# Kernel tuning notes

Measured on AMD Instinct MI355X. Metric: run time of the kernel, lower is better.

Reference implementation:

```python
import jax, jax.numpy as jnp
import numpy as np
from jax.scipy.special import gammaln, xlogy

DIM = 1536
HEADS = 8
DK = 64
DV = 64
BS = 128
N = 1536
NRPF = 192  # num_rel_pos_features, divisible by 6
B = 2


def _positional_embed(n, feat):
    # [2n-1, feat] relative positional basis (exponential, central-mask, gamma),
    # each duplicated with sign(d) asymmetric variant.
    f = feat // 6
    d = jnp.arange(-n + 1, n, dtype=jnp.float32)
    ad = jnp.abs(d)[:, None]  # [2n-1, 1]
    # exponential: log-spaced half lives
    half_life = 2.0 ** jnp.linspace(3.0, float(np.log2(n)), f)
    e_exp = jnp.exp(-float(np.log(2.0)) / half_life[None, :] * ad)
    # central mask: 1 if |d| < 2^i - 1
    widths = 2.0 ** jnp.arange(1, f + 1, dtype=jnp.float32) - 1.0
    e_cm = (widths[None, :] > ad).astype(jnp.float32)
    # gamma pdf, linearly spaced means
    std = n / (2.0 * f)
    mean = jnp.linspace(n / f, float(n), f)[None, :]
    conc = (mean / std) ** 2
    rate = mean / (std ** 2)
    log_unnorm = xlogy(conc - 1.0, ad) - rate * ad
    log_norm = gammaln(conc) - conc * jnp.log(rate)
    probs = jnp.exp(log_unnorm - log_norm) + 1e-8
    e_g = probs / jnp.max(probs, axis=-1, keepdims=True)
    emb = jnp.concatenate([e_exp, e_cm, e_g], axis=-1)  # [2n-1, 3f]
    return jnp.concatenate([emb, jnp.sign(d)[:, None] * emb], axis=-1)  # [2n-1, 6f]


def _relative_shift(t):
    # [B, H, N, 2N-1] -> [B, H, N, N] (Transformer-XL shift)
    b, h, t1, t2 = t.shape
    t = jnp.concatenate([jnp.zeros_like(t[..., :1]), t], axis=-1)  # [.., t2+1]
    t = t.reshape(b, h, t2 + 1, t1)[:, :, 1:, :].reshape(b, h, t1, t2)
    return t[..., :t1]


def setup_inputs() -> dict:
    key = jax.random.key(0)
    ks = jax.random.split(key, 10)
    x = jax.random.normal(ks[0], (B, N, DIM), dtype=jnp.float32)
    Wq = jax.random.normal(ks[1], (DIM, HEADS * DK), dtype=jnp.float32) * 0.02
    Wk = jax.random.normal(ks[2], (DIM, HEADS * DK), dtype=jnp.float32) * 0.02
    Wv = jax.random.normal(ks[3], (DIM, HEADS * DV), dtype=jnp.float32) * 0.02
    Wrel = jax.random.normal(ks[4], (NRPF, HEADS * DK), dtype=jnp.float32) * 0.02
    rel_content_bias = jax.random.normal(ks[5], (1, HEADS, 1, DK), dtype=jnp.float32)
    rel_pos_bias = jax.random.normal(ks[6], (1, HEADS, 1, DK), dtype=jnp.float32)
    # to_out is zero-init in the original; use small random so the output/grads are non-trivial
    Wo = jax.random.normal(ks[7], (HEADS * DV, DIM), dtype=jnp.float32) * 0.02
    bo = jnp.zeros((DIM,), dtype=jnp.float32)
    pos_embed = _positional_embed(N, NRPF)  # [2N-1, NRPF]
    # BigBird block-local window mask: blocks bi attend to blocks bi-1..bi+1
    bi = np.arange(N) // BS
    local_mask = jnp.asarray(np.abs(bi[:, None] - bi[None, :]) <= 1)  # [N, N] bool
    # a few global tokens per batch
    is_global = jnp.zeros((B, N), dtype=bool).at[:, :4].set(True)
    return {"x": x, "Wq": Wq, "Wk": Wk, "Wv": Wv, "Wrel": Wrel,
            "rel_content_bias": rel_content_bias, "rel_pos_bias": rel_pos_bias,
            "Wo": Wo, "bo": bo, "pos_embed": pos_embed,
            "local_mask": local_mask, "is_global": is_global}


def reference(x, Wq, Wk, Wv, Wrel, rel_content_bias, rel_pos_bias, Wo, bo,
              pos_embed, local_mask, is_global):
    b, n, _ = x.shape
    h, dk = rel_content_bias.shape[1], rel_content_bias.shape[-1]
    dv = Wv.shape[-1] // h
    scale = dk ** -0.5
    q = (x @ Wq).reshape(b, n, h, dk).transpose(0, 2, 1, 3) * scale  # [b,h,n,dk]
    k = (x @ Wk).reshape(b, n, h, dk).transpose(0, 2, 1, 3)
    v = (x @ Wv).reshape(b, n, h, dv).transpose(0, 2, 1, 3)
    content_logits = jnp.einsum('bhid,bhjd->bhij', q + rel_content_bias, k)
    rel_k = (pos_embed @ Wrel).reshape(2 * n - 1, h, dk).transpose(1, 0, 2)  # [h,2n-1,dk]
    rel_logits = jnp.einsum('bhid,hjd->bhij', q + rel_pos_bias, rel_k)  # [b,h,n,2n-1]
    logits = content_logits + _relative_shift(rel_logits)
    attn_bool = (local_mask[None, None] | is_global[:, None, :, None]
                 | is_global[:, None, None, :])
    logits = jnp.where(attn_bool, logits.astype(jnp.float32), -jnp.inf)
    attn = jax.nn.softmax(logits, axis=-1)
    out = jnp.einsum('bhij,bhjd->bhid', attn, v.astype(jnp.float32))
    out = out.astype(x.dtype).transpose(0, 2, 1, 3).reshape(b, n, h * dv)
    return out @ Wo + bo
```

## Files before the change

kernel.cpp:

```cpp
#include <hip/hip_runtime.h>
#include <math.h>

#define NSEQ 1536
#define HD3  1536
#define RKLD 512
#define RLEN 3071
#define NB   12

typedef __attribute__((ext_vector_type(8))) short bf16x8;
typedef __attribute__((ext_vector_type(4))) float f32x4;
typedef _Float16 f16x8 __attribute__((ext_vector_type(8)));
typedef _Float16 f16x4 __attribute__((ext_vector_type(4)));

__device__ __forceinline__ unsigned short f2bf(float f) {
    union { float f; unsigned u; } v; v.f = f;
    unsigned r = v.u + 0x7fffu + ((v.u >> 16) & 1u);
    return (unsigned short)(r >> 16);
}
__device__ __forceinline__ float bf2f(unsigned short s) {
    union { unsigned u; float f; } v; v.u = ((unsigned)s) << 16;
    return v.f;
}
__device__ __forceinline__ unsigned short f2h(float f) {
    union { _Float16 h; unsigned short u; } c; c.h = (_Float16)f; return c.u;
}
__device__ __forceinline__ void cp16(const void* g, void* l) {
    __builtin_amdgcn_global_load_lds(
        (const __attribute__((address_space(1))) void*)g,
        (__attribute__((address_space(3))) void*)l, 16, 0, 0);
}

#define KSWZ(row, d) ((row) * 64 + (((((d) >> 3) ^ ((row) & 7))) << 3) + ((d) & 7))
#define PSWZ(r, j)   ((r) * 128 + (((((j) >> 3) ^ ((r) & 15))) << 3) + ((j) & 7))
#define VSTR 136

__global__ __launch_bounds__(256) void split2_f16(
    const float* __restrict__ X, _Float16* __restrict__ HX,
    const float* __restrict__ P, _Float16* __restrict__ HP)
{
    const int bid = blockIdx.x;
    const float* src; _Float16* dst; int i;
    if (bid < 4608) {
        i = bid * 256 + threadIdx.x;
        src = X; dst = HX;
    } else {
        i = (bid - 4608) * 256 + threadIdx.x;
        if (i >= 147408) return;
        src = P; dst = HP;
    }
    float4 v = ((const float4*)src)[i];
    union { _Float16 h[4]; ushort4 u; } c;
    c.h[0] = (_Float16)v.x; c.h[1] = (_Float16)v.y;
    c.h[2] = (_Float16)v.z; c.h[3] = (_Float16)v.w;
    ((ushort4*)dst)[i] = c.u;
}

__device__ __forceinline__ void wsplit_body16(
    const float* __restrict__ W, _Float16* __restrict__ T,
    int K, int N, int n_off, int ldt, float scale, int bx, int by)
{
    __shared__ float tile[64][65];
    const int k0 = by * 64, n0 = bx * 64;
    const int t = threadIdx.x;
    const int rr = t >> 4, c4 = (t & 15) * 4;
#pragma unroll
    for (int p = 0; p < 4; ++p) {
        int r = p * 16 + rr;
        float4 v = *(const float4*)(W + (size_t)(k0 + r) * N + n0 + c4);
        tile[r][c4 + 0] = v.x; tile[r][c4 + 1] = v.y;
        tile[r][c4 + 2] = v.z; tile[r][c4 + 3] = v.w;
    }
    __syncthreads();
#pragma unroll
    for (int p = 0; p < 4; ++p) {
        int n = p * 16 + rr;
        union { _Float16 h[4]; ushort4 u; } cc;
        cc.h[0] = (_Float16)(tile[c4 + 0][n] * scale);
        cc.h[1] = (_Float16)(tile[c4 + 1][n] * scale);
        cc.h[2] = (_Float16)(tile[c4 + 2][n] * scale);
        cc.h[3] = (_Float16)(tile[c4 + 3][n] * scale);
        size_t o = (size_t)(n_off + n0 + n) * ldt + k0 + c4;
        *(ushort4*)(T + o) = cc.u;
    }
}

__global__ __launch_bounds__(256) void wsplit_all(
    const float* __restrict__ Wq, const float* __restrict__ Wk,
    const float* __restrict__ Wv, const float* __restrict__ Wo,
    const float* __restrict__ Wrel,
    _Float16* __restrict__ Tqkv, _Float16* __restrict__ To,
    _Float16* __restrict__ Trel)
{
    const int z = blockIdx.z;
    if (z < 3) {
        const float* W = (z == 0) ? Wq : (z == 1) ? Wk : Wv;
        wsplit_body16(W, Tqkv, 1536, 512, z * 512, 1536,
                      (z == 0) ? 0.125f : 1.f, blockIdx.x, blockIdx.y);
    } else if (z == 3) {
        wsplit_body16(Wo, To, 512, 1536, 0, 512, 1.f, blockIdx.y, blockIdx.x);
    } else {
        if (blockIdx.y >= 3) return;
        wsplit_body16(Wrel, Trel, 192, 512, 0, 192, 1.f, blockIdx.x, blockIdx.y);
    }
}

__global__ __launch_bounds__(256) void gemm_f16k(
    const _Float16* __restrict__ A,
    const _Float16* __restrict__ B,
    const float* __restrict__ bias, void* __restrict__ C,
    int M, int N, int K, int omode)
{
    __shared__ _Float16 sA[2][4096];
    __shared__ _Float16 sB[2][4096];
    const int t = threadIdx.x;
    const int wave = t >> 6, lane = t & 63;
    const int nwg = gridDim.x * gridDim.y;
    const int lin = blockIdx.y * gridDim.x + blockIdx.x;
    const int swz = (lin & 7) * (nwg >> 3) + (lin >> 3);
    const int bx = swz % gridDim.x, by = swz / gridDim.x;
    const int m0 = by * 64, n0 = bx * 64;
    const int wm = (wave >> 1) * 32, wn = (wave & 1) * 32;
    const int fr = lane & 15, quad = lane >> 4;

    f32x4 acc[2][2];
#pragma unroll
    for (int i = 0; i < 2; ++i)
#pragma unroll
        for (int j = 0; j < 2; ++j)
#pragma unroll
            for (int c = 0; c < 4; ++c) acc[i][j][c] = 0.f;

    const int nsteps = K >> 6;

#define STAGE(k0, buf)                                                        \
    {                                                                         \
        _Pragma("unroll")                                                     \
        for (int it = 0; it < 2; ++it) {                                      \
            int cidx = it * 256 + t;                                          \
            int row = cidx >> 3, slot = cidx & 7;                             \
            int gch = slot ^ (row & 7);                                       \
            size_t goA = (size_t)(m0 + row) * K + (k0) + gch * 8;             \
            size_t goB = (size_t)(n0 + row) * K + (k0) + gch * 8;             \
            cp16(A + goA, &sA[buf][it * 2048 + wave * 512]);                  \
            cp16(B + goB, &sB[buf][it * 2048 + wave * 512]);                  \
        }                                                                     \
    }

    STAGE(0, 0);
    for (int s = 0; s < nsteps; ++s) {
        const int buf = s & 1;
        __syncthreads();
        if (s + 1 < nsteps) STAGE((s + 1) * 64, buf ^ 1);

        f16x8 fa[2][2], fb[2][2];
#pragma unroll
        for (int ti = 0; ti < 2; ++ti)
#pragma unroll
            for (int kc = 0; kc < 2; ++kc) {
                fa[ti][kc] = *(const f16x8*)&sA[buf][KSWZ(wm + ti * 16 + fr,
                                                          kc * 32 + quad * 8)];
                fb[ti][kc] = *(const f16x8*)&sB[buf][KSWZ(wn + ti * 16 + fr,
                                                          kc * 32 + quad * 8)];
            }
#pragma unroll
        for (int ti = 0; ti < 2; ++ti)
#pragma unroll
            for (int tj = 0; tj < 2; ++tj)
#pragma unroll
                for (int kc = 0; kc < 2; ++kc)
                    acc[ti][tj] = __builtin_amdgcn_mfma_f32_16x16x32_f16(
                        fa[ti][kc], fb[tj][kc], acc[ti][tj], 0, 0, 0);
    }
#undef STAGE

    if (omode == 0) {
        float* Cf = (float*)C;
#pragma unroll
        for (int ti = 0; ti < 2; ++ti) {
            int rowb = m0 + wm + ti * 16 + quad * 4;
#pragma unroll
            for (int tj = 0; tj < 2; ++tj) {
                int col = n0 + wn + tj * 16 + fr;
                float bb = bias ? bias[col] : 0.f;
#pragma unroll
                for (int j2 = 0; j2 < 4; ++j2)
                    Cf[(size_t)(rowb + j2) * N + col] = acc[ti][tj][j2] + bb;
            }
        }
    } else {
        unsigned short* Cu = (unsigned short*)C;
        const bool vb = (omode == 1) && (n0 >= 1024);
#pragma unroll
        for (int ti = 0; ti < 2; ++ti) {
            int rowb = m0 + wm + ti * 16 + quad * 4;
#pragma unroll
            for (int tj = 0; tj < 2; ++tj) {
                int col = n0 + wn + tj * 16 + fr;
#pragma unroll
                for (int j2 = 0; j2 < 4; ++j2) {
                    float v = acc[ti][tj][j2];
                    Cu[(size_t)(rowb + j2) * N + col] = vb ? f2bf(v) : f2h(v);
                }
            }
        }
    }
}

__global__ __launch_bounds__(256) void drk_kernel(
    const _Float16* __restrict__ rkh, const float* __restrict__ cb,
    const float* __restrict__ rb, float* __restrict__ drk)
{
    int idx = blockIdx.x * 256 + threadIdx.x;
    if (idx >= 8 * RLEN) return;
    int jj = idx >> 3, h = idx & 7;
    const _Float16* rrow = rkh + (size_t)jj * RKLD + h * 64;
    float s0 = 0, s1 = 0, s2 = 0, s3 = 0;
#pragma unroll
    for (int d4 = 0; d4 < 16; ++d4) {
        f16x4 rv = *(const f16x4*)(rrow + d4 * 4);
        float dx = rb[h * 64 + d4 * 4 + 0] - cb[h * 64 + d4 * 4 + 0];
        float dy = rb[h * 64 + d4 * 4 + 1] - cb[h * 64 + d4 * 4 + 1];
        float dz = rb[h * 64 + d4 * 4 + 2] - cb[h * 64 + d4 * 4 + 2];
        float dw = rb[h * 64 + d4 * 4 + 3] - cb[h * 64 + d4 * 4 + 3];
        s0 = fmaf(dx, (float)rv[0], s0); s1 = fmaf(dy, (float)rv[1], s1);
        s2 = fmaf(dz, (float)rv[2], s2); s3 = fmaf(dw, (float)rv[3], s3);
    }
    drk[h * RLEN + jj] = (s0 + s1) + (s2 + s3);
}

__global__ __launch_bounds__(256) void relb_mfma(
    const _Float16* __restrict__ qkvh, const _Float16* __restrict__ rkh,
    const float* __restrict__ rb, _Float16* __restrict__ relbT)
{
    __shared__ _Float16 sR[8192];
    const int ct = blockIdx.x, bi = blockIdx.y, bh = blockIdx.z;
    const int b = bh >> 3, h = bh & 7;
    const int i0 = bi * 128;
    const int c0 = (bi == 0) ? 0 : (bi - 1) * 128;
    const int jjbase = c0 - i0 - 127 + (NSEQ - 1) + ct * 128;
    const int t = threadIdx.x;
    const int wave = t >> 6, lane = t & 63;
    const int fr = lane & 15, quad = lane >> 4;

    {
        const _Float16* Rg = rkh + (size_t)jjbase * RKLD + h * 64;
#pragma unroll
        for (int it = 0; it < 4; ++it) {
            int cidx = it * 256 + t;
            int row = cidx >> 3, slot = cidx & 7;
            int gch = slot ^ (row & 7);
            cp16(Rg + (size_t)row * RKLD + gch * 8,
                 &sR[it * 2048 + wave * 512]);
        }
    }
    f16x8 qf[2][2];
    {
        const _Float16* Qg = qkvh + ((size_t)(b * NSEQ + i0)) * HD3 + h * 64;
#pragma unroll
        for (int ti = 0; ti < 2; ++ti)
#pragma unroll
            for (int kc = 0; kc < 2; ++kc) {
                int m = wave * 32 + ti * 16 + fr;
                int k8 = kc * 32 + quad * 8;
                f16x8 qv = *(const f16x8*)(Qg + (size_t)m * HD3 + k8);
                const float* cp = rb + h * 64 + k8;
                _Float16 hx[8];
#pragma unroll
                for (int u = 0; u < 8; ++u)
                    hx[u] = (_Float16)((float)qv[u] + cp[u]);
                qf[ti][kc] = *(f16x8*)hx;
            }
    }
    __syncthreads();

    f32x4 sacc[2][8];
#pragma unroll
    for (int i = 0; i < 2; ++i)
#pragma unroll
        for (int j = 0; j < 8; ++j)
#pragma unroll
            for (int c = 0; c < 4; ++c) sacc[i][j][c] = 0.f;

#pragma unroll
    for (int kc = 0; kc < 2; ++kc) {
        f16x8 bv[8];
#pragma unroll
        for (int tj = 0; tj < 8; ++tj)
            bv[tj] = *(const f16x8*)&sR[KSWZ(tj * 16 + fr, kc * 32 + quad * 8)];
#pragma unroll
        for (int ti = 0; ti < 2; ++ti)
#pragma unroll
            for (int tj = 0; tj < 8; ++tj)
                sacc[ti][tj] = __builtin_amdgcn_mfma_f32_16x16x32_f16(
                    qf[ti][kc], bv[tj], sacc[ti][tj], 0, 0, 0);
    }

    size_t bb_ = ((size_t)bh * NB + bi) * 512;
#pragma unroll
    for (int ti = 0; ti < 2; ++ti) {
        int mr = wave * 32 + ti * 16 + quad * 4;
#pragma unroll
        for (int tj = 0; tj < 8; ++tj) {
            int ccg = ct * 128 + tj * 16 + fr;
#pragma unroll
            for (int reg = 0; reg < 4; ++reg) {
                int r = mr + reg;
                int jl = ccg - 127 + r;
                if (jl >= 0)
                    relbT[(bb_ + jl) * 128 + r] = (_Float16)sacc[ti][tj][reg];
            }
        }
    }
}

__global__ __launch_bounds__(256) void attn_mfma(
    const _Float16* __restrict__ qkvh, const _Float16* __restrict__ relbT,
    const _Float16* __restrict__ rkh, const float* __restrict__ drk,
    const float* __restrict__ cb, float* __restrict__ O_part,
    float* __restrict__ l_part)
{
    __shared__ unsigned short sKP[16384];
    __shared__ unsigned short sVt[64 * VSTR];
    __shared__ float p_g[128 * 4];
    __shared__ __align__(16) float vg[4 * 64];
    __shared__ float lg[128];
    const int ct = blockIdx.x, bi = blockIdx.y, bh = blockIdx.z;
    const int b = bh >> 3, h = bh & 7;
    const int i0 = bi * 128;
    const int c0 = (bi == 0) ? 0 : (bi - 1) * 128;
    const int c1 = (bi == NB - 1) ? NSEQ : (bi + 2) * 128;
    const int ctile = c0 + ct * 128;
    const int t = threadIdx.x;
    const int wave = t >> 6, lane = t & 63;
    const int fr = lane & 15, quad = lane >> 4;

    float* Op = O_part + (((size_t)ct * 16 + bh) * NSEQ + i0) * 64;
    float* lp = l_part + ((size_t)ct * 16 + bh) * NSEQ + i0;

    if (ctile >= c1) {
        for (int k2 = t; k2 < 8192; k2 += 256) Op[k2] = 0.f;
        if (t < 128) lp[t] = 0.f;
        return;
    }

    const bool do_g = (ct == 0 && bi >= 2);
    const unsigned short* Vall = (const unsigned short*)qkvh;

    {
        const _Float16* Kg = qkvh + ((size_t)(b * NSEQ + ctile)) * HD3 + 512 + h * 64;
#pragma unroll
        for (int it = 0; it < 4; ++it) {
            int cidx = it * 256 + t;
            int row = cidx >> 3, slot = cidx & 7;
            int gch = slot ^ (row & 7);
            cp16(Kg + (size_t)row * HD3 + gch * 8,
                 (unsigned short*)&sKP[it * 2048 + wave * 512]);
        }
    }
    {
        const unsigned short* Vg = Vall + ((size_t)(b * NSEQ + ctile)) * HD3
                                   + 1024 + h * 64;
#pragma unroll
        for (int it = 0; it < 2; ++it) {
            int lin = it * 256 + t;
            int r4 = (lin >> 4) * 4, d4 = (lin & 15) * 4;
            ushort4 v0 = *(const ushort4*)(Vg + (size_t)(r4 + 0) * HD3 + d4);
            ushort4 v1 = *(const ushort4*)(Vg + (size_t)(r4 + 1) * HD3 + d4);
            ushort4 v2 = *(const ushort4*)(Vg + (size_t)(r4 + 2) * HD3 + d4);
            ushort4 v3 = *(const ushort4*)(Vg + (size_t)(r4 + 3) * HD3 + d4);
            const unsigned short* p0 = (const unsigned short*)&v0;
            const unsigned short* p1 = (const unsigned short*)&v1;
            const unsigned short* p2 = (const unsigned short*)&v2;
            const unsigned short* p3 = (const unsigned short*)&v3;
#pragma unroll
            for (int dd = 0; dd < 4; ++dd) {
                ushort4 hh;
                hh.x = p0[dd]; hh.y = p1[dd]; hh.z = p2[dd]; hh.w = p3[dd];
                *(ushort4*)&sVt[(d4 + dd) * VSTR + r4] = hh;
            }
        }
    }
    if (do_g) {
        if (t < 128) {
            const int r = t;
            const int i = i0 + r;
            const int jjb = NSEQ - 1 - i;
            const _Float16* qrow = qkvh + (size_t)(b * NSEQ + i) * HD3 + h * 64;
            const _Float16* krow = qkvh + (size_t)(b * NSEQ) * HD3 + 512 + h * 64;
            const _Float16* rrow = rkh + (size_t)jjb * RKLD + h * 64;
            float s[4] = {0.f, 0.f, 0.f, 0.f};
#pragma unroll
            for (int d4 = 0; d4 < 16; ++d4) {
                f16x4 qv = *(const f16x4*)(qrow + d4 * 4);
                float4 cv = *(const float4*)(cb + h * 64 + d4 * 4);
                float q0 = (float)qv[0] + cv.x, q1 = (float)qv[1] + cv.y;
                float q2 = (float)qv[2] + cv.z, q3 = (float)qv[3] + cv.w;
#pragma unroll
                for (int j = 0; j < 4; ++j) {
                    f16x4 kv = *(const f16x4*)(krow + (size_t)j * HD3 + d4 * 4);
                    f16x4 rv = *(const f16x4*)(rrow + (size_t)j * RKLD + d4 * 4);
                    s[j] = fmaf(q0, (float)kv[0] + (float)rv[0], s[j]);
                    s[j] = fmaf(q1, (float)kv[1] + (float)rv[1], s[j]);
                    s[j] = fmaf(q2, (float)kv[2] + (float)rv[2], s[j]);
                    s[j] = fmaf(q3, (float)kv[3] + (float)rv[3], s[j]);
                }
            }
            float l = 0.f;
#pragma unroll
            for (int j = 0; j < 4; ++j) {
                float p = __expf(s[j] + drk[h * RLEN + jjb + j]);
                p_g[r * 4 + j] = p;
                l += p;
            }
            lg[r] = l;
        } else {
            const unsigned short* Vg0 = Vall + (size_t)(b * NSEQ) * HD3
                                        + 1024 + h * 64;
            int u = (t - 128) * 2;
#pragma unroll
            for (int w = 0; w < 2; ++w) {
                int idx = u + w;
                vg[idx] = bf2f(Vg0[(size_t)(idx >> 6) * HD3 + (idx & 63)]);
            }
        }
    }
    f16x8 qf[2][2];
    {
        const _Float16* Qg = qkvh + ((size_t)(b * NSEQ + i0)) * HD3 + h * 64;
#pragma unroll
        for (int ti = 0; ti < 2; ++ti)
#pragma unroll
            for (int kc = 0; kc < 2; ++kc) {
                int m = wave * 32 + ti * 16 + fr;
                int k8 = kc * 32 + quad * 8;
                f16x8 qv = *(const f16x8*)(Qg + (size_t)m * HD3 + k8);
                const float* cp = cb + h * 64 + k8;
                _Float16 hx[8];
#pragma unroll
                for (int u = 0; u < 8; ++u)
                    hx[u] = (_Float16)((float)qv[u] + cp[u]);
                qf[ti][kc] = *(f16x8*)hx;
            }
    }
    __syncthreads();

    f32x4 sacc[2][8];
#pragma unroll
    for (int i = 0; i < 2; ++i)
#pragma unroll
        for (int j = 0; j < 8; ++j)
#pragma unroll
            for (int c = 0; c < 4; ++c) sacc[i][j][c] = 0.f;

#pragma unroll
    for (int kc = 0; kc < 2; ++kc) {
        f16x8 bv[8];
#pragma unroll
        for (int tj = 0; tj < 8; ++tj)
            bv[tj] = *(const f16x8*)&sKP[KSWZ(tj * 16 + fr, kc * 32 + quad * 8)];
#pragma unroll
        for (int ti = 0; ti < 2; ++ti)
#pragma unroll
            for (int tj = 0; tj < 8; ++tj)
                sacc[ti][tj] = __builtin_amdgcn_mfma_f32_16x16x32_f16(
                    qf[ti][kc], bv[tj], sacc[ti][tj], 0, 0, 0);
    }
    __syncthreads();

    const _Float16* relbase = relbT + (((size_t)bh * NB + bi) * 512 + ct * 128) * 128;
    float lsum[2][4] = {{0.f, 0.f, 0.f, 0.f}, {0.f, 0.f, 0.f, 0.f}};
#pragma unroll
    for (int ti = 0; ti < 2; ++ti) {
        int mr = wave * 32 + ti * 16 + quad * 4;
#pragma unroll
        for (int tj = 0; tj < 8; ++tj) {
            int j = tj * 16 + fr;
            f16x4 rl = *(const f16x4*)&relbase[(size_t)j * 128 + mr];
#pragma unroll
            for (int reg = 0; reg < 4; ++reg) {
                int r = mr + reg;
                float p = __expf(sacc[ti][tj][reg] + (float)rl[reg]);
                unsigned short pb = f2bf(p);
                lsum[ti][reg] += bf2f(pb);
                sKP[PSWZ(r, j)] = pb;
            }
        }
    }
#pragma unroll
    for (int m2 = 1; m2 < 16; m2 <<= 1)
#pragma unroll
        for (int ti = 0; ti < 2; ++ti)
#pragma unroll
            for (int reg = 0; reg < 4; ++reg)
                lsum[ti][reg] += __shfl_xor(lsum[ti][reg], m2, 64);
    if (fr == 0) {
#pragma unroll
        for (int ti = 0; ti < 2; ++ti) {
            int mr = wave * 32 + ti * 16 + quad * 4;
#pragma unroll
            for (int reg = 0; reg < 4; ++reg)
                lp[mr + reg] = lsum[ti][reg] + (do_g ? lg[mr + reg] : 0.f);
        }
    }

    f32x4 oacc[4][2];
#pragma unroll
    for (int i = 0; i < 4; ++i)
#pragma unroll
        for (int j = 0; j < 2; ++j)
#pragma unroll
            for (int c = 0; c < 4; ++c) oacc[i][j][c] = 0.f;

#pragma unroll
    for (int kc = 0; kc < 4; ++kc) {
        bf16x8 pbv[2];
#pragma unroll
        for (int rt2 = 0; rt2 < 2; ++rt2) {
            int r = (wave * 2 + rt2) * 16 + fr;
            pbv[rt2] = *(const bf16x8*)&sKP[PSWZ(r, kc * 32 + quad * 8)];
        }
#pragma unroll
        for (int dt = 0; dt < 4; ++dt) {
            bf16x8 av = *(const bf16x8*)&sVt[(dt * 16 + fr) * VSTR + kc * 32 + quad * 8];
#pragma unroll
            for (int rt2 = 0; rt2 < 2; ++rt2)
                oacc[dt][rt2] = __builtin_amdgcn_mfma_f32_16x16x32_bf16(
                    av, pbv[rt2], oacc[dt][rt2], 0, 0, 0);
        }
    }
#pragma unroll
    for (int rt2 = 0; rt2 < 2; ++rt2) {
        int r = (wave * 2 + rt2) * 16 + fr;
        float pg0 = 0.f, pg1 = 0.f, pg2 = 0.f, pg3 = 0.f;
        if (do_g) {
            pg0 = p_g[r * 4 + 0]; pg1 = p_g[r * 4 + 1];
            pg2 = p_g[r * 4 + 2]; pg3 = p_g[r * 4 + 3];
        }
#pragma unroll
        for (int dt = 0; dt < 4; ++dt) {
            int d = dt * 16 + quad * 4;
            float4 ov = make_float4(oacc[dt][rt2][0], oacc[dt][rt2][1],
                                    oacc[dt][rt2][2], oacc[dt][rt2][3]);
            if (do_g) {
                float4 v0 = *(const float4*)&vg[0 * 64 + d];
                float4 v1 = *(const float4*)&vg[1 * 64 + d];
                float4 v2 = *(const float4*)&vg[2 * 64 + d];
                float4 v3 = *(const float4*)&vg[3 * 64 + d];
                ov.x += pg0 * v0.x + pg1 * v1.x + pg2 * v2.x + pg3 * v3.x;
                ov.y += pg0 * v0.y + pg1 * v1.y + pg2 * v2.y + pg3 * v3.y;
                ov.z += pg0 * v0.z + pg1 * v1.z + pg2 * v2.z + pg3 * v3.z;
                ov.w += pg0 * v0.w + pg1 * v1.w + pg2 * v2.w + pg3 * v3.w;
            }
            *(float4*)(Op + (size_t)r * 64 + d) = ov;
        }
    }
}

__global__ __launch_bounds__(256) void grows_part(
    const _Float16* __restrict__ qkvh, const _Float16* __restrict__ rkh,
    const float* __restrict__ drk, const float* __restrict__ cb,
    float* __restrict__ g_O, float* __restrict__ g_l)
{
    __shared__ float qc_s[64];
    __shared__ float p_s[128];
    __shared__ float obuf[4][64];
    __shared__ float lred[2];
    const int chunk = blockIdx.x;
    const int bhi = blockIdx.y;
    const int i = bhi & 3, h = (bhi >> 2) & 7, b = bhi >> 5;
    const int t = threadIdx.x;
    const int c0 = chunk * 128;
    if (t < 64)
        qc_s[t] = (float)qkvh[(size_t)(b * NSEQ + i) * HD3 + h * 64 + t]
                  + cb[h * 64 + t];
    __syncthreads();
    if (t < 128) {
        int j = c0 + t;
        const _Float16* krow = qkvh + (size_t)(b * NSEQ + j) * HD3 + 512 + h * 64;
        int jj = j - i + (NSEQ - 1);
        const _Float16* rrow = rkh + (size_t)jj * RKLD + h * 64;
        float s0 = 0, s1 = 0, s2 = 0, s3 = 0;
#pragma unroll
        for (int d4 = 0; d4 < 16; ++d4) {
            f16x4 kv = *(const f16x4*)(krow + d4 * 4);
            f16x4 rv = *(const f16x4*)(rrow + d4 * 4);
            float4 qv = *(const float4*)(&qc_s[d4 * 4]);
            s0 = fmaf(qv.x, (float)kv[0] + (float)rv[0], s0);
            s1 = fmaf(qv.y, (float)kv[1] + (float)rv[1], s1);
            s2 = fmaf(qv.z, (float)kv[2] + (float)rv[2], s2);
            s3 = fmaf(qv.w, (float)kv[3] + (float)rv[3], s3);
        }
        float p = __expf((s0 + s1) + (s2 + s3) + drk[h * RLEN + jj]);
        p_s[t] = p;
        float ls = p;
#pragma unroll
        for (int off = 32; off > 0; off >>= 1)
            ls += __shfl_down(ls, off, 64);
        if ((t & 63) == 0) lred[t >> 6] = ls;
    }
    __syncthreads();
    {
        const int d = t & 63, g = t >> 6;
        float a0 = 0, a1 = 0;
        const unsigned short* vbase = (const unsigned short*)qkvh
            + (size_t)(b * NSEQ + c0 + g * 32) * HD3 + 1024 + h * 64 + d;
#pragma unroll
        for (int j2 = 0; j2 < 32; j2 += 2) {
            a0 = fmaf(p_s[g * 32 + j2],     bf2f(vbase[(size_t)j2 * HD3]),       a0);
            a1 = fmaf(p_s[g * 32 + j2 + 1], bf2f(vbase[(size_t)(j2 + 1) * HD3]), a1);
        }
        obuf[g][d] = a0 + a1;
    }
    __syncthreads();
    if (t < 64) {
        float o = (obuf[0][t] + obuf[1][t]) + (obuf[2][t] + obuf[3][t]);
        g_O[((size_t)chunk * 64 + bhi) * 64 + t] = o;
        if (t == 0) g_l[chunk * 64 + bhi] = lred[0] + lred[1];
    }
}

__global__ __launch_bounds__(256) void norm_merge(
    const float* __restrict__ O_part, const float* __restrict__ l_part,
    const float* __restrict__ g_O, const float* __restrict__ g_l,
    _Float16* __restrict__ aoh)
{
    const int bh = blockIdx.y, b = bh >> 3, h = bh & 7;
    const int i = blockIdx.x * 16 + (threadIdx.x >> 4);
    const int d4 = threadIdx.x & 15;
    float ox = 0, oy = 0, oz = 0, ow = 0, l = 0;
    if (i < 4) {
        const int bhi = bh * 4 + i;
#pragma unroll
        for (int c = 0; c < 12; ++c) {
            const float* gp = g_O + ((size_t)c * 64 + bhi) * 64 + d4 * 4;
            ox += gp[0]; oy += gp[1]; oz += gp[2]; ow += gp[3];
            l += g_l[c * 64 + bhi];
        }
    } else {
#pragma unroll
        for (int s = 0; s < 3; ++s) {
            const float* Opp = O_part + (((size_t)s * 16 + bh) * NSEQ + i) * 64 + d4 * 4;
            float4 p = *(const float4*)Opp;
            ox += p.x; oy += p.y; oz += p.z; ow += p.w;
            l += l_part[((size_t)s * 16 + bh) * NSEQ + i];
        }
    }
    float inv = 1.f / l;
    union { _Float16 h[4]; ushort4 u; } cc;
    cc.h[0] = (_Float16)(ox * inv); cc.h[1] = (_Float16)(oy * inv);
    cc.h[2] = (_Float16)(oz * inv); cc.h[3] = (_Float16)(ow * inv);
    size_t o = ((size_t)(b * NSEQ + i)) * 512 + h * 64 + d4 * 4;
    *(ushort4*)(aoh + o) = cc.u;
}

extern "C" void kernel_launch(void* const* d_in, const int* in_sizes, int n_in,
                              void* d_out, int out_size, void* d_ws, size_t ws_size,
                              hipStream_t stream)
{
    const float* x    = (const float*)d_in[0];
    const float* Wq   = (const float*)d_in[1];
    const float* Wk   = (const float*)d_in[2];
    const float* Wv   = (const float*)d_in[3];
    const float* Wrel = (const float*)d_in[4];
    const float* cb   = (const float*)d_in[5];
    const float* rb   = (const float*)d_in[6];
    const float* Wo   = (const float*)d_in[7];
    const float* bo   = (const float*)d_in[8];
    const float* pe   = (const float*)d_in[9];
    float* out = (float*)d_out;

    float* ws = (float*)d_ws;
    _Float16* qkvh = (_Float16*)ws;
    _Float16* rkh  = (_Float16*)(ws + 2359296);
    float* drk   = ws + 3145728;
    _Float16* aoh = (_Float16*)(ws + 3170304);
    _Float16* woh = (_Float16*)(ws + 3956736);
    float* R = ws + 4349952;
    _Float16* relbT = (_Float16*)R;
    _Float16* xh  = (_Float16*)R;
    _Float16* wqh = (_Float16*)(R + 2359296);
    float* g_O = R + 6291456;
    float* g_l = R + 6340608;
    float* O_part = ws + 10691328;
    float* l_part = ws + 15409920;
    _Float16* peh   = (_Float16*)(ws + 15483648);
    _Float16* wrelT = (_Float16*)(ws + 15778560);

    dim3 blk(256);
    split2_f16<<<5184, blk, 0, stream>>>(x, xh, pe, peh);
    wsplit_all<<<dim3(8, 24, 5), blk, 0, stream>>>(Wq, Wk, Wv, Wo, Wrel,
                                                   wqh, woh, wrelT);
    gemm_f16k<<<dim3(24, 48), blk, 0, stream>>>(xh, wqh, nullptr, qkvh,
                                                3072, 1536, 1536, 1);
    gemm_f16k<<<dim3(8, 48), blk, 0, stream>>>(peh, wrelT, nullptr, rkh,
                                               3072, 512, 192, 2);
    drk_kernel<<<96, blk, 0, stream>>>(rkh, cb, rb, drk);
    relb_mfma<<<dim3(4, 12, 16), blk, 0, stream>>>(qkvh, rkh, rb, relbT);
    attn_mfma<<<dim3(3, 12, 16), blk, 0, stream>>>(qkvh, relbT, rkh, drk, cb,
                                                   O_part, l_part);
    grows_part<<<dim3(12, 64), blk, 0, stream>>>(qkvh, rkh, drk, cb, g_O, g_l);
    norm_merge<<<dim3(96, 16), blk, 0, stream>>>(O_part, l_part, g_O, g_l, aoh);
    gemm_f16k<<<dim3(24, 48), blk, 0, stream>>>(aoh, woh, bo, out,
                                                3072, 1536, 512, 0);
}
```

Before: 227.3 us.

## Loop over key tiles inside attention block and fuse normalization into output

The attention kernel used to split each query tile across three key-column tiles, each writing fp32 partial outputs and row sums that a separate merge kernel combined. It now loops over the two or three column tiles inside one block, accumulating O and the row sums in registers, then normalizes and writes fp16 output directly. A small kernel patches only the first four global rows. This removes the partial-buffer traffic and the merge pass, at the cost of fewer blocks (192 instead of 576) and less parallelism on the GPU.

```diff
diff --git a/kernel.cpp b/kernel.cpp
--- a/kernel.cpp
+++ b/kernel.cpp
@@ -313,73 +313,29 @@
     }
 }
 
-__global__ __launch_bounds__(256) void attn_mfma(
+__global__ __launch_bounds__(256) void attn_flash(
     const _Float16* __restrict__ qkvh, const _Float16* __restrict__ relbT,
     const _Float16* __restrict__ rkh, const float* __restrict__ drk,
-    const float* __restrict__ cb, float* __restrict__ O_part,
-    float* __restrict__ l_part)
+    const float* __restrict__ cb, _Float16* __restrict__ aoh)
 {
     __shared__ unsigned short sKP[16384];
     __shared__ unsigned short sVt[64 * VSTR];
     __shared__ float p_g[128 * 4];
     __shared__ __align__(16) float vg[4 * 64];
     __shared__ float lg[128];
-    const int ct = blockIdx.x, bi = blockIdx.y, bh = blockIdx.z;
+    __shared__ float lrow[128];
+    const int bi = blockIdx.x, bh = blockIdx.y;
     const int b = bh >> 3, h = bh & 7;
     const int i0 = bi * 128;
     const int c0 = (bi == 0) ? 0 : (bi - 1) * 128;
     const int c1 = (bi == NB - 1) ? NSEQ : (bi + 2) * 128;
-    const int ctile = c0 + ct * 128;
+    const int nt = (c1 - c0) >> 7;
     const int t = threadIdx.x;
     const int wave = t >> 6, lane = t & 63;
     const int fr = lane & 15, quad = lane >> 4;
-
-    float* Op = O_part + (((size_t)ct * 16 + bh) * NSEQ + i0) * 64;
-    float* lp = l_part + ((size_t)ct * 16 + bh) * NSEQ + i0;
-
-    if (ctile >= c1) {
-        for (int k2 = t; k2 < 8192; k2 += 256) Op[k2] = 0.f;
-        if (t < 128) lp[t] = 0.f;
-        return;
-    }
-
-    const bool do_g = (ct == 0 && bi >= 2);
+    const bool do_g = (bi >= 2);
     const unsigned short* Vall = (const unsigned short*)qkvh;
 
-    {
-        const _Float16* Kg = qkvh + ((size_t)(b * NSEQ + ctile)) * HD3 + 512 + h * 64;
-#pragma unroll
-        for (int it = 0; it < 4; ++it) {
-            int cidx = it * 256 + t;
-            int row = cidx >> 3, slot = cidx & 7;
-            int gch = slot ^ (row & 7);
-            cp16(Kg + (size_t)row * HD3 + gch * 8,
-                 (unsigned short*)&sKP[it * 2048 + wave * 512]);
-        }
-    }
-    {
-        const unsigned short* Vg = Vall + ((size_t)(b * NSEQ + ctile)) * HD3
-                                   + 1024 + h * 64;
-#pragma unroll
-        for (int it = 0; it < 2; ++it) {
-            int lin = it * 256 + t;
-            int r4 = (lin >> 4) * 4, d4 = (lin & 15) * 4;
-            ushort4 v0 = *(const ushort4*)(Vg + (size_t)(r4 + 0) * HD3 + d4);
-            ushort4 v1 = *(const ushort4*)(Vg + (size_t)(r4 + 1) * HD3 + d4);
-            ushort4 v2 = *(const ushort4*)(Vg + (size_t)(r4 + 2) * HD3 + d4);
-            ushort4 v3 = *(const ushort4*)(Vg + (size_t)(r4 + 3) * HD3 + d4);
-            const unsigned short* p0 = (const unsigned short*)&v0;
-            const unsigned short* p1 = (const unsigned short*)&v1;
-            const unsigned short* p2 = (const unsigned short*)&v2;
-            const unsigned short* p3 = (const unsigned short*)&v3;
-#pragma unroll
-            for (int dd = 0; dd < 4; ++dd) {
-                ushort4 hh;
-                hh.x = p0[dd]; hh.y = p1[dd]; hh.z = p2[dd]; hh.w = p3[dd];
-                *(ushort4*)&sVt[(d4 + dd) * VSTR + r4] = hh;
-            }
-        }
-    }
     if (do_g) {
         if (t < 128) {
             const int r = t;
@@ -442,50 +398,120 @@
                 qf[ti][kc] = *(f16x8*)hx;
             }
     }
-    __syncthreads();
-
-    f32x4 sacc[2][8];
-#pragma unroll
-    for (int i = 0; i < 2; ++i)
-#pragma unroll
-        for (int j = 0; j < 8; ++j)
-#pragma unroll
-            for (int c = 0; c < 4; ++c) sacc[i][j][c] = 0.f;
-
-#pragma unroll
-    for (int kc = 0; kc < 2; ++kc) {
-        f16x8 bv[8];
-#pragma unroll
-        for (int tj = 0; tj < 8; ++tj)
-            bv[tj] = *(const f16x8*)&sKP[KSWZ(tj * 16 + fr, kc * 32 + quad * 8)];
-#pragma unroll
-        for (int ti = 0; ti < 2; ++ti)
+
+    f32x4 oacc[4][2];
+#pragma unroll
+    for (int i = 0; i < 4; ++i)
+#pragma unroll
+        for (int j = 0; j < 2; ++j)
+#pragma unroll
+            for (int c = 0; c < 4; ++c) oacc[i][j][c] = 0.f;
+    float lsum[2][4] = {{0.f, 0.f, 0.f, 0.f}, {0.f, 0.f, 0.f, 0.f}};
+
+    for (int ct = 0; ct < nt; ++ct) {
+        const int ctile = c0 + ct * 128;
+        {
+            const _Float16* Kg = qkvh + ((size_t)(b * NSEQ + ctile)) * HD3
+                                 + 512 + h * 64;
+#pragma unroll
+            for (int it = 0; it < 4; ++it) {
+                int cidx = it * 256 + t;
+                int row = cidx >> 3, slot = cidx & 7;
+                int gch = slot ^ (row & 7);
+                cp16(Kg + (size_t)row * HD3 + gch * 8,
+                     (unsigned short*)&sKP[it * 2048 + wave * 512]);
+            }
+        }
+        {
+            const unsigned short* Vg = Vall + ((size_t)(b * NSEQ + ctile)) * HD3
+                                       + 1024 + h * 64;
+#pragma unroll
+            for (int it = 0; it < 2; ++it) {
+                int lin = it * 256 + t;
+                int r4 = (lin >> 4) * 4, d4 = (lin & 15) * 4;
+                ushort4 v0 = *(const ushort4*)(Vg + (size_t)(r4 + 0) * HD3 + d4);
+                ushort4 v1 = *(const ushort4*)(Vg + (size_t)(r4 + 1) * HD3 + d4);
+                ushort4 v2 = *(const ushort4*)(Vg + (size_t)(r4 + 2) * HD3 + d4);
+                ushort4 v3 = *(const ushort4*)(Vg + (size_t)(r4 + 3) * HD3 + d4);
+                const unsigned short* p0 = (const unsigned short*)&v0;
+                const unsigned short* p1 = (const unsigned short*)&v1;
+                const unsigned short* p2 = (const unsigned short*)&v2;
+                const unsigned short* p3 = (const unsigned short*)&v3;
+#pragma unroll
+                for (int dd = 0; dd < 4; ++dd) {
+                    ushort4 hh;
+                    hh.x = p0[dd]; hh.y = p1[dd]; hh.z = p2[dd]; hh.w = p3[dd];
+                    *(ushort4*)&sVt[(d4 + dd) * VSTR + r4] = hh;
+                }
+            }
+        }
+        __syncthreads();
+
+        f32x4 sacc[2][8];
+#pragma unroll
+        for (int i = 0; i < 2; ++i)
+#pragma unroll
+            for (int j = 0; j < 8; ++j)
+#pragma unroll
+                for (int c = 0; c < 4; ++c) sacc[i][j][c] = 0.f;
+
+#pragma unroll
+        for (int kc = 0; kc < 2; ++kc) {
+            f16x8 bv[8];
 #pragma unroll
             for (int tj = 0; tj < 8; ++tj)
-                sacc[ti][tj] = __builtin_amdgcn_mfma_f32_16x16x32_f16(
-                    qf[ti][kc], bv[tj], sacc[ti][tj], 0, 0, 0);
-    }
-    __syncthreads();
-
-    const _Float16* relbase = relbT + (((size_t)bh * NB + bi) * 512 + ct * 128) * 128;
-    float lsum[2][4] = {{0.f, 0.f, 0.f, 0.f}, {0.f, 0.f, 0.f, 0.f}};
-#pragma unroll
-    for (int ti = 0; ti < 2; ++ti) {
-        int mr = wave * 32 + ti * 16 + quad * 4;
-#pragma unroll
-        for (int tj = 0; tj < 8; ++tj) {
-            int j = tj * 16 + fr;
-            f16x4 rl = *(const f16x4*)&relbase[(size_t)j * 128 + mr];
-#pragma unroll
-            for (int reg = 0; reg < 4; ++reg) {
-                int r = mr + reg;
-                float p = __expf(sacc[ti][tj][reg] + (float)rl[reg]);
-                unsigned short pb = f2bf(p);
-                lsum[ti][reg] += bf2f(pb);
-                sKP[PSWZ(r, j)] = pb;
-            }
-        }
-    }
+                bv[tj] = *(const f16x8*)&sKP[KSWZ(tj * 16 + fr,
+                                                  kc * 32 + quad * 8)];
+#pragma unroll
+            for (int ti = 0; ti < 2; ++ti)
+#pragma unroll
+                for (int tj = 0; tj < 8; ++tj)
+                    sacc[ti][tj] = __builtin_amdgcn_mfma_f32_16x16x32_f16(
+                        qf[ti][kc], bv[tj], sacc[ti][tj], 0, 0, 0);
+        }
+        __syncthreads();
+
+        const _Float16* relbase = relbT
+            + (((size_t)bh * NB + bi) * 512 + ct * 128) * 128;
+#pragma unroll
+        for (int ti = 0; ti < 2; ++ti) {
+            int mr = wave * 32 + ti * 16 + quad * 4;
+#pragma unroll
+            for (int tj = 0; tj < 8; ++tj) {
+                int j = tj * 16 + fr;
+                f16x4 rl = *(const f16x4*)&relbase[(size_t)j * 128 + mr];
+#pragma unroll
+                for (int reg = 0; reg < 4; ++reg) {
+                    int r = mr + reg;
+                    float p = __expf(sacc[ti][tj][reg] + (float)rl[reg]);
+                    unsigned short pb = f2bf(p);
+                    lsum[ti][reg] += bf2f(pb);
+                    sKP[PSWZ(r, j)] = pb;
+                }
+            }
+        }
+
+#pragma unroll
+        for (int kc = 0; kc < 4; ++kc) {
+            bf16x8 pbv[2];
+#pragma unroll
+            for (int rt2 = 0; rt2 < 2; ++rt2) {
+                int r = (wave * 2 + rt2) * 16 + fr;
+                pbv[rt2] = *(const bf16x8*)&sKP[PSWZ(r, kc * 32 + quad * 8)];
+            }
+#pragma unroll
+            for (int dt = 0; dt < 4; ++dt) {
+                bf16x8 av = *(const bf16x8*)&sVt[(dt * 16 + fr) * VSTR
+                                                 + kc * 32 + quad * 8];
+#pragma unroll
+                for (int rt2 = 0; rt2 < 2; ++rt2)
+                    oacc[dt][rt2] = __builtin_amdgcn_mfma_f32_16x16x32_bf16(
+                        av, pbv[rt2], oacc[dt][rt2], 0, 0, 0);
+            }
+        }
+        __syncthreads();
+    }
+
 #pragma unroll
     for (int m2 = 1; m2 < 16; m2 <<= 1)
 #pragma unroll
@@ -499,43 +525,22 @@
             int mr = wave * 32 + ti * 16 + quad * 4;
 #pragma unroll
             for (int reg = 0; reg < 4; ++reg)
-                lp[mr + reg] = lsum[ti][reg] + (do_g ? lg[mr + reg] : 0.f);
-        }
-    }
-
-    f32x4 oacc[4][2];
-#pragma unroll
-    for (int i = 0; i < 4; ++i)
-#pragma unroll
-        for (int j = 0; j < 2; ++j)
-#pragma unroll
-            for (int c = 0; c < 4; ++c) oacc[i][j][c] = 0.f;
-
-#pragma unroll
-    for (int kc = 0; kc < 4; ++kc) {
-        bf16x8 pbv[2];
-#pragma unroll
-        for (int rt2 = 0; rt2 < 2; ++rt2) {
-            int r = (wave * 2 + rt2) * 16 + fr;
-            pbv[rt2] = *(const bf16x8*)&sKP[PSWZ(r, kc * 32 + quad * 8)];
-        }
-#pragma unroll
-        for (int dt = 0; dt < 4; ++dt) {
-            bf16x8 av = *(const bf16x8*)&sVt[(dt * 16 + fr) * VSTR + kc * 32 + quad * 8];
-#pragma unroll
-            for (int rt2 = 0; rt2 < 2; ++rt2)
-                oacc[dt][rt2] = __builtin_amdgcn_mfma_f32_16x16x32_bf16(
-                    av, pbv[rt2], oacc[dt][rt2], 0, 0, 0);
-        }
-    }
+                lrow[mr + reg] = lsum[ti][reg];
+        }
+    }
+    __syncthreads();
+
 #pragma unroll
     for (int rt2 = 0; rt2 < 2; ++rt2) {
         int r = (wave * 2 + rt2) * 16 + fr;
+        float l = lrow[r] + (do_g ? lg[r] : 0.f);
+        float linv = 1.f / l;
         float pg0 = 0.f, pg1 = 0.f, pg2 = 0.f, pg3 = 0.f;
         if (do_g) {
             pg0 = p_g[r * 4 + 0]; pg1 = p_g[r * 4 + 1];
             pg2 = p_g[r * 4 + 2]; pg3 = p_g[r * 4 + 3];
         }
+        _Float16* arow = aoh + ((size_t)(b * NSEQ + i0 + r)) * 512 + h * 64;
 #pragma unroll
         for (int dt = 0; dt < 4; ++dt) {
             int d = dt * 16 + quad * 4;
@@ -551,7 +556,10 @@
                 ov.z += pg0 * v0.z + pg1 * v1.z + pg2 * v2.z + pg3 * v3.z;
                 ov.w += pg0 * v0.w + pg1 * v1.w + pg2 * v2.w + pg3 * v3.w;
             }
-            *(float4*)(Op + (size_t)r * 64 + d) = ov;
+            union { _Float16 h[4]; ushort4 u; } cc;
+            cc.h[0] = (_Float16)(ov.x * linv); cc.h[1] = (_Float16)(ov.y * linv);
+            cc.h[2] = (_Float16)(ov.z * linv); cc.h[3] = (_Float16)(ov.w * linv);
+            *(ushort4*)(arow + d) = cc.u;
         }
     }
 }
@@ -619,38 +627,20 @@
     }
 }
 
-__global__ __launch_bounds__(256) void norm_merge(
-    const float* __restrict__ O_part, const float* __restrict__ l_part,
+__global__ __launch_bounds__(256) void gfix(
     const float* __restrict__ g_O, const float* __restrict__ g_l,
     _Float16* __restrict__ aoh)
 {
-    const int bh = blockIdx.y, b = bh >> 3, h = bh & 7;
-    const int i = blockIdx.x * 16 + (threadIdx.x >> 4);
-    const int d4 = threadIdx.x & 15;
-    float ox = 0, oy = 0, oz = 0, ow = 0, l = 0;
-    if (i < 4) {
-        const int bhi = bh * 4 + i;
-#pragma unroll
-        for (int c = 0; c < 12; ++c) {
-            const float* gp = g_O + ((size_t)c * 64 + bhi) * 64 + d4 * 4;
-            ox += gp[0]; oy += gp[1]; oz += gp[2]; ow += gp[3];
-            l += g_l[c * 64 + bhi];
-        }
-    } else {
-#pragma unroll
-        for (int s = 0; s < 3; ++s) {
-            const float* Opp = O_part + (((size_t)s * 16 + bh) * NSEQ + i) * 64 + d4 * 4;
-            float4 p = *(const float4*)Opp;
-            ox += p.x; oy += p.y; oz += p.z; ow += p.w;
-            l += l_part[((size_t)s * 16 + bh) * NSEQ + i];
-        }
-    }
-    float inv = 1.f / l;
-    union { _Float16 h[4]; ushort4 u; } cc;
-    cc.h[0] = (_Float16)(ox * inv); cc.h[1] = (_Float16)(oy * inv);
-    cc.h[2] = (_Float16)(oz * inv); cc.h[3] = (_Float16)(ow * inv);
-    size_t o = ((size_t)(b * NSEQ + i)) * 512 + h * 64 + d4 * 4;
-    *(ushort4*)(aoh + o) = cc.u;
+    const int bh = blockIdx.x, b = bh >> 3, h = bh & 7;
+    const int i = threadIdx.x >> 6, d = threadIdx.x & 63;
+    const int bhi = bh * 4 + i;
+    float o = 0.f, l = 0.f;
+#pragma unroll
+    for (int c = 0; c < 12; ++c) {
+        o += g_O[((size_t)c * 64 + bhi) * 64 + d];
+        l += g_l[c * 64 + bhi];
+    }
+    aoh[((size_t)(b * NSEQ + i)) * 512 + h * 64 + d] = (_Float16)(o / l);
 }
 
 extern "C" void kernel_launch(void* const* d_in, const int* in_sizes, int n_in,
@@ -681,8 +671,6 @@
     _Float16* wqh = (_Float16*)(R + 2359296);
     float* g_O = R + 6291456;
     float* g_l = R + 6340608;
-    float* O_part = ws + 10691328;
-    float* l_part = ws + 15409920;
     _Float16* peh   = (_Float16*)(ws + 15483648);
     _Float16* wrelT = (_Float16*)(ws + 15778560);
 
@@ -696,10 +684,9 @@
                                                3072, 512, 192, 2);
     drk_kernel<<<96, blk, 0, stream>>>(rkh, cb, rb, drk);
     relb_mfma<<<dim3(4, 12, 16), blk, 0, stream>>>(qkvh, rkh, rb, relbT);
-    attn_mfma<<<dim3(3, 12, 16), blk, 0, stream>>>(qkvh, relbT, rkh, drk, cb,
-                                                   O_part, l_part);
+    attn_flash<<<dim3(12, 16), blk, 0, stream>>>(qkvh, relbT, rkh, drk, cb, aoh);
     grows_part<<<dim3(12, 64), blk, 0, stream>>>(qkvh, rkh, drk, cb, g_O, g_l);
-    norm_merge<<<dim3(96, 16), blk, 0, stream>>>(O_part, l_part, g_O, g_l, aoh);
+    gfix<<<16, blk, 0, stream>>>(g_O, g_l, aoh);
     gemm_f16k<<<dim3(24, 48), blk, 0, stream>>>(aoh, woh, bo, out,
                                                 3072, 1536, 512, 0);
 }
```

Result: no change. 231.1 us (+1.7%).
